# Performance work log

Hardware: AMD Instinct MI355X
Metric: run time of the kernel (lower is better)

Reference implementation:

```python
import jax, jax.numpy as jnp
import numpy as np

TOKENS, D_IN = 8192, 1024
E, D_OUT = 8, 1024
H = 2 * D_OUT  # Expert hidden = 2 * num_outputs


def setup_inputs() -> dict:
    key = jax.random.key(0)
    ks = jax.random.split(key, 4)
    s_in = 1.0 / np.sqrt(D_IN)
    s_h = 1.0 / np.sqrt(H)
    return {
        "x": jax.random.normal(ks[0], (TOKENS, D_IN), dtype=jnp.float32),
        "W1": jax.random.normal(ks[1], (E, D_IN, H), dtype=jnp.float32) * s_in,
        "b1": jnp.zeros((E, H), dtype=jnp.float32),
        "W2": jax.random.normal(ks[2], (E, H, D_OUT), dtype=jnp.float32) * s_h,
        "b2": jnp.zeros((E, D_OUT), dtype=jnp.float32),
        "Wg": jax.random.normal(ks[3], (D_IN, E), dtype=jnp.float32) * s_in,
        "bg": jnp.zeros((E,), dtype=jnp.float32),
    }


def reference(x, W1, b1, W2, b2, Wg, bg):
    # Gating: softmax over experts. gates: [N, E]
    gates = jax.nn.softmax(x @ Wg + bg, axis=-1)
    # All experts run densely: batched GEMM over expert axis.
    h = jax.nn.relu(jnp.einsum('nd,edh->neh', x, W1) + b1)       # [N, E, H]
    expert_out = jnp.einsum('neh,ehf->nef', h, W2) + b2          # [N, E, D_OUT]
    # Gate-weighted sum over experts (fused stack*gate->sum).
    return jnp.einsum('nef,ne->nf', expert_out, gates)            # [N, D_OUT]
```

## Files before the change

kernel.cpp:

```cpp
#include <hip/hip_runtime.h>
#include <stdint.h>

#define TOKENS 8192
#define D_IN   1024
#define NEXP   8
#define D_OUT  1024
#define HDIM   2048

typedef __bf16 bf16x8 __attribute__((ext_vector_type(8)));
typedef __bf16 bf16x4 __attribute__((ext_vector_type(4)));
typedef float  f32x4  __attribute__((ext_vector_type(4)));

__device__ __forceinline__ void gload16(const void* g, void* l) {
  __builtin_amdgcn_global_load_lds(
      (const __attribute__((address_space(1))) void*)g,
      (__attribute__((address_space(3))) void*)l,
      16, 0, 0);
}

template <int N>
__device__ __forceinline__ void waitv() {
  if constexpr (N == 0)      asm volatile("s_waitcnt vmcnt(0)" ::: "memory");
  else if constexpr (N == 1) asm volatile("s_waitcnt vmcnt(1)" ::: "memory");
  else if constexpr (N == 2) asm volatile("s_waitcnt vmcnt(2)" ::: "memory");
  else if constexpr (N == 3) asm volatile("s_waitcnt vmcnt(3)" ::: "memory");
  else if constexpr (N == 4) asm volatile("s_waitcnt vmcnt(4)" ::: "memory");
  else static_assert(N <= 4, "unsupported vmcnt");
}

__global__ void gate_cvt_kernel(const float* __restrict__ x,
                                const float* __restrict__ Wg,
                                const float* __restrict__ bg,
                                float* __restrict__ gates,
                                __bf16* __restrict__ xb) {
  const int lane = threadIdx.x & 63;
  const int n = blockIdx.x * 4 + (threadIdx.x >> 6);
  float acc[NEXP];
#pragma unroll
  for (int e = 0; e < NEXP; ++e) acc[e] = 0.f;
  const float* xr = x + (size_t)n * D_IN;
  __bf16* xo = xb + (size_t)n * D_IN;
#pragma unroll 4
  for (int d0 = 0; d0 < D_IN; d0 += 64) {
    const int d = d0 + lane;
    float xv = xr[d];
    xo[d] = (__bf16)xv;
    const float* wr = Wg + d * NEXP;
#pragma unroll
    for (int e = 0; e < NEXP; ++e) acc[e] += xv * wr[e];
  }
#pragma unroll
  for (int e = 0; e < NEXP; ++e) {
    float v = acc[e];
#pragma unroll
    for (int off = 32; off > 0; off >>= 1) v += __shfl_down(v, off);
    acc[e] = v;
  }
  if (lane == 0) {
    float mx = -1e30f;
#pragma unroll
    for (int e = 0; e < NEXP; ++e) { acc[e] += bg[e]; mx = fmaxf(mx, acc[e]); }
    float s = 0.f;
#pragma unroll
    for (int e = 0; e < NEXP; ++e) { acc[e] = expf(acc[e] - mx); s += acc[e]; }
    float inv = 1.f / s;
#pragma unroll
    for (int e = 0; e < NEXP; ++e) gates[n * NEXP + e] = acc[e] * inv;
  }
}

__global__ void transpose_cvt_kernel(const float* __restrict__ W,
                                     __bf16* __restrict__ Wt,
                                     int K, int N, int EPG) {
  __shared__ float tile[32][33];
  const int e = blockIdx.z;
  const int ldo = EPG * K;
  const float* Win = W + (size_t)e * K * N;
  __bf16* Wout = Wt + (size_t)(e / EPG) * N * ldo + (size_t)(e % EPG) * K;
  const int n0 = blockIdx.x * 32;
  const int k0 = blockIdx.y * 32;
  const int tx = threadIdx.x & 31;
  const int ty = threadIdx.x >> 5;
#pragma unroll
  for (int r = ty; r < 32; r += 8)
    tile[r][tx] = Win[(size_t)(k0 + r) * N + n0 + tx];
  __syncthreads();
#pragma unroll
  for (int r = ty; r < 32; r += 8)
    Wout[(size_t)(n0 + r) * ldo + k0 + tx] = (__bf16)tile[tx][r];
}

__global__ void merge_kernel(float* __restrict__ out,
                             const float* __restrict__ gates,
                             const float* __restrict__ b2) {
  const int idx = blockIdx.x * 256 + threadIdx.x;
  const int n = idx >> 8;
  const int fb = idx & 255;
  float4 o = ((const float4*)out)[idx];
  const float* g = gates + (size_t)n * NEXP;
#pragma unroll
  for (int e = 0; e < NEXP; ++e) {
    const float ge = g[e];
    float4 b = ((const float4*)(b2 + (size_t)e * D_OUT))[fb];
    o.x += ge * b.x; o.y += ge * b.y; o.z += ge * b.z; o.w += ge * b.w;
  }
  ((float4*)out)[idx] = o;
}

template <int NT, int WPE, int BM, int BN, int WM, int WN, int EPI>
__global__ __launch_bounds__(NT, WPE)
void moe_gemm(const __bf16* __restrict__ A, size_t AZ,
              const __bf16* __restrict__ B, size_t BZ,
              const float* __restrict__ b1g,
              const float* __restrict__ gates,
              int e0,
              __bf16* __restrict__ Hout, int OCZ, int ldo,
              float* __restrict__ F0,
              int first, int M, int N, int K) {
  constexpr int RM = BM / WM, RN = BN / WN;
  constexpr int FM = RM / 16, FN = RN / 16;
  constexpr int HM = FM / 2,  HN = FN / 2;
  constexpr int LA = BM * 4 / NT;
  constexpr int LB = BN * 4 / NT;
  constexpr int AELEM = BM * 64;
  static_assert(HM >= 1 && HN >= 1, "tile too small");
  __shared__ alignas(16) __bf16 lds[(BM + BN) * 64];

  const int tid  = threadIdx.x;
  const int lane = tid & 63;
  const int wave = tid >> 6;
  const int wr   = wave / WN;
  const int wc   = wave % WN;
  const int lrow = lane & 15;
  const int khi  = lane >> 4;
  const int sx   = (lrow & 7) << 3;
  const int bz   = blockIdx.z;

  A += (size_t)bz * AZ;
  B += (size_t)bz * BZ;

  const int Gx   = gridDim.x;
  const int nwg  = Gx * gridDim.y;
  const int orig = blockIdx.y * Gx + blockIdx.x;
  const int wgid = (orig & 7) * (nwg >> 3) + (orig >> 3);
  const int bn0  = (wgid % Gx) * BN;
  const int bm0  = (wgid / Gx) * BM;

  const __bf16* srcA[2][LA];
  const __bf16* srcB[2][LB];
#pragma unroll
  for (int q = 0; q < 2; ++q) {
#pragma unroll
    for (int j = 0; j < LA; ++j) {
      int o   = q * (BM * 64) + j * (NT * 16) + tid * 16;
      int row = o >> 7;
      int cb  = (o & 127) ^ ((row & 7) << 4);
      srcA[q][j] = A + (size_t)(bm0 + row) * K + (cb >> 1);
    }
#pragma unroll
    for (int j = 0; j < LB; ++j) {
      int o   = q * (BN * 64) + j * (NT * 16) + tid * 16;
      int row = o >> 7;
      int cb  = (o & 127) ^ ((row & 7) << 4);
      srcB[q][j] = B + (size_t)(bn0 + row) * K + (cb >> 1);
    }
  }

  auto stageA = [&](int kt, int q) {
#pragma unroll
    for (int j = 0; j < LA; ++j)
      gload16(srcA[q][j] + (size_t)kt * 64,
              lds + q * (BM * 32) + j * (NT * 8) + wave * 512);
  };
  auto stageB = [&](int kt, int q) {
#pragma unroll
    for (int j = 0; j < LB; ++j)
      gload16(srcB[q][j] + (size_t)kt * 64,
              lds + AELEM + q * (BN * 32) + j * (NT * 8) + wave * 512);
  };

  f32x4 acc[FM][FN];
#pragma unroll
  for (int m = 0; m < FM; ++m)
#pragma unroll
    for (int n = 0; n < FN; ++n) acc[m][n] = f32x4{0.f, 0.f, 0.f, 0.f};

  bf16x8 af[HM][2];
  bf16x8 bf[2][HN][2];

  auto rdA = [&](int mq) {
#pragma unroll
    for (int mi = 0; mi < HM; ++mi)
#pragma unroll
      for (int kk = 0; kk < 2; ++kk)
        af[mi][kk] = *(const bf16x8*)
            &lds[(size_t)(mq * (BM / 2) + wr * (RM / 2) + mi * 16 + lrow) * 64 +
                 ((kk * 32 + khi * 8) ^ sx)];
  };
  auto rdB = [&](int nq) {
#pragma unroll
    for (int ni = 0; ni < HN; ++ni)
#pragma unroll
      for (int kk = 0; kk < 2; ++kk)
        bf[nq][ni][kk] = *(const bf16x8*)
            &lds[AELEM +
                 (size_t)(nq * (BN / 2) + wc * (RN / 2) + ni * 16 + lrow) * 64 +
                 ((kk * 32 + khi * 8) ^ sx)];
  };
  auto cluster = [&](int mq, int nq) {
    __builtin_amdgcn_s_setprio(1);
#pragma unroll
    for (int kk = 0; kk < 2; ++kk)
#pragma unroll
      for (int mi = 0; mi < HM; ++mi)
#pragma unroll
        for (int ni = 0; ni < HN; ++ni)
          acc[mq * HM + mi][nq * HN + ni] =
              __builtin_amdgcn_mfma_f32_16x16x32_bf16(
                  af[mi][kk], bf[nq][ni][kk], acc[mq * HM + mi][nq * HN + ni],
                  0, 0, 0);
    __builtin_amdgcn_s_setprio(0);
  };

#define BAR()   asm volatile("s_barrier" ::: "memory")
#define LGKM0() do { asm volatile("s_waitcnt lgkmcnt(0)" ::: "memory"); \
                     __builtin_amdgcn_sched_barrier(0); } while (0)

  const int nk = K >> 6;

  stageA(0, 0); stageB(0, 0); stageB(0, 1);
  waitv<LB>();
  BAR();

  for (int t = 0; t < nk; ++t) {
    const bool pf = (t + 1 < nk);

    rdA(0); rdB(0);
    stageA(t, 1);
    BAR(); LGKM0();
    cluster(0, 0);
    waitv<LA>();
    BAR();
    rdB(1);
    if (pf) stageA(t + 1, 0);
    BAR(); LGKM0();
    cluster(0, 1);
    if (pf) waitv<LA>(); else waitv<0>();
    BAR();
    rdA(1);
    if (pf) stageB(t + 1, 0);
    BAR(); LGKM0();
    cluster(1, 0);
    BAR();
    if (pf) stageB(t + 1, 1);
    BAR();
    cluster(1, 1);
    if (pf) waitv<LB>();
    BAR();
  }

#undef BAR
#undef LGKM0

  const float* bias = (EPI == 0) ? b1g + (size_t)(e0 + bz) * HDIM : nullptr;
  const int ecol = e0 + bz;
  __bf16* Hp = (EPI == 0) ? Hout + (size_t)bz * OCZ : nullptr;

#pragma unroll
  for (int m = 0; m < FM; ++m) {
    const int grow0 = bm0 + (m / HM) * (BM / 2) + wr * (RM / 2) +
                      (m % HM) * 16 + khi * 4;
    if constexpr (EPI == 0) {
      float g[4];
#pragma unroll
      for (int r = 0; r < 4; ++r)
        g[r] = gates[(size_t)(grow0 + r) * NEXP + ecol];
#pragma unroll
      for (int n = 0; n < FN; ++n) {
        const int gcol = bn0 + (n / HN) * (BN / 2) + wc * (RN / 2) +
                         (n % HN) * 16 + lrow;
        const float bv = bias[gcol];
        f32x4 a = acc[m][n];
#pragma unroll
        for (int r = 0; r < 4; ++r) {
          float v = a[r] + bv;
          v = v > 0.f ? v : 0.f;
          Hp[(size_t)(grow0 + r) * ldo + gcol] = (__bf16)(v * g[r]);
        }
      }
    } else {
#pragma unroll
      for (int n = 0; n < FN; ++n) {
        const int gcol = bn0 + (n / HN) * (BN / 2) + wc * (RN / 2) +
                         (n % HN) * 16 + lrow;
        f32x4 a = acc[m][n];
#pragma unroll
        for (int r = 0; r < 4; ++r) {
          float* o = F0 + (size_t)(grow0 + r) * N + gcol;
          if (first) *o = a[r];
          else       *o += a[r];
        }
      }
    }
  }
}

extern "C" void kernel_launch(void* const* d_in, const int* in_sizes, int n_in,
                              void* d_out, int out_size, void* d_ws, size_t ws_size,
                              hipStream_t stream) {
  const float* x  = (const float*)d_in[0];
  const float* W1 = (const float*)d_in[1];
  const float* b1 = (const float*)d_in[2];
  const float* W2 = (const float*)d_in[3];
  const float* b2 = (const float*)d_in[4];
  const float* Wg = (const float*)d_in[5];
  const float* bg = (const float*)d_in[6];
  float* out = (float*)d_out;

  char* w = (char*)d_ws;
  float* gates = (float*)w;   w += (size_t)TOKENS * NEXP * 4;
  __bf16* xb   = (__bf16*)w;  w += (size_t)TOKENS * D_IN * 2;
  __bf16* w1t  = (__bf16*)w;  w += (size_t)NEXP * HDIM * D_IN * 2;
  __bf16* w2c  = (__bf16*)w;  w += (size_t)NEXP * D_OUT * HDIM * 2;
  const size_t base = (size_t)(w - (char*)d_ws);

  const size_t h1_b = (size_t)TOKENS * HDIM * 2;
  const int G = (ws_size >= base + 4 * h1_b) ? 4
              : (ws_size >= base + 2 * h1_b) ? 2 : 1;
  __bf16* hbuf = (__bf16*)w;

  const size_t WSLICE = (size_t)HDIM * D_IN;
  const int KB = G * HDIM;

  gate_cvt_kernel<<<TOKENS / 4, 256, 0, stream>>>(x, Wg, bg, gates, xb);
  transpose_cvt_kernel<<<dim3(HDIM / 32, D_IN / 32, NEXP), 256, 0, stream>>>(
      W1, w1t, D_IN, HDIM, 1);
  transpose_cvt_kernel<<<dim3(D_OUT / 32, HDIM / 32, NEXP), 256, 0, stream>>>(
      W2, w2c, HDIM, D_OUT, G);

  const int ngroups = NEXP / G;
  for (int d = 0; d < ngroups; ++d) {
    if (G >= 2) {
      for (int i2 = 0; i2 < G / 2; ++i2) {
        const int e0 = G * d + 2 * i2;
        moe_gemm<512, 2, 256, 256, 2, 4, 0><<<dim3(8, 32, 2), 512, 0, stream>>>(
            xb, 0, w1t + (size_t)e0 * WSLICE, WSLICE, b1, gates, e0,
            hbuf + (size_t)i2 * 2 * HDIM, HDIM, KB,
            nullptr, 0, TOKENS, HDIM, D_IN);
      }
    } else {
      moe_gemm<512, 2, 256, 256, 2, 4, 0><<<dim3(8, 32, 1), 512, 0, stream>>>(
          xb, 0, w1t + (size_t)d * WSLICE, 0, b1, gates, d,
          hbuf, 0, KB,
          nullptr, 0, TOKENS, HDIM, D_IN);
    }
    moe_gemm<256, 3, 128, 128, 2, 2, 3><<<dim3(D_OUT / 128, TOKENS / 128, 1),
                                          256, 0, stream>>>(
        hbuf, 0, w2c + (size_t)d * D_OUT * KB, 0,
        nullptr, nullptr, 0, nullptr, 0, 0,
        out, (d == 0) ? 1 : 0, TOKENS, D_OUT, KB);
  }

  merge_kernel<<<TOKENS, 256, 0, stream>>>(out, gates, b2);
}
```

Before: 645.5 us.

## Use register-staged double-buffered LDS pipeline for second MoE GEMM

Adds an RSTG variant of the GEMM used for the second (hidden-to-output) matmul. It loads tiles two k-steps ahead into registers and writes them into a double-buffered LDS slot, replacing direct global-to-LDS loads. This drops to one barrier per k-step instead of many. It also cuts that kernel's occupancy hint from 3 to 2 workgroups per CU, and the doubled LDS and extra registers (16 float4 staging values) may limit occupancy.

New measurement: 653.9 us. About the same (+1.3%).

```diff
diff --git a/kernel.cpp b/kernel.cpp
--- a/kernel.cpp
+++ b/kernel.cpp
@@ -25,7 +25,8 @@
   else if constexpr (N == 2) asm volatile("s_waitcnt vmcnt(2)" ::: "memory");
   else if constexpr (N == 3) asm volatile("s_waitcnt vmcnt(3)" ::: "memory");
   else if constexpr (N == 4) asm volatile("s_waitcnt vmcnt(4)" ::: "memory");
-  else static_assert(N <= 4, "unsupported vmcnt");
+  else if constexpr (N == 8) asm volatile("s_waitcnt vmcnt(8)" ::: "memory");
+  else static_assert(N <= 8, "unsupported vmcnt");
 }
 
 __global__ void gate_cvt_kernel(const float* __restrict__ x,
@@ -107,7 +108,7 @@
   ((float4*)out)[idx] = o;
 }
 
-template <int NT, int WPE, int BM, int BN, int WM, int WN, int EPI>
+template <int NT, int WPE, int BM, int BN, int WM, int WN, int EPI, int RSTG>
 __global__ __launch_bounds__(NT, WPE)
 void moe_gemm(const __bf16* __restrict__ A, size_t AZ,
               const __bf16* __restrict__ B, size_t BZ,
@@ -123,8 +124,10 @@
   constexpr int LA = BM * 4 / NT;
   constexpr int LB = BN * 4 / NT;
   constexpr int AELEM = BM * 64;
+  constexpr int SLOT  = (BM + BN) * 64;
+  constexpr int NSLOT = (RSTG == 0) ? 1 : 2;
   static_assert(HM >= 1 && HN >= 1, "tile too small");
-  __shared__ alignas(16) __bf16 lds[(BM + BN) * 64];
+  __shared__ alignas(16) __bf16 lds[NSLOT * SLOT];
 
   const int tid  = threadIdx.x;
   const int lane = tid & 63;
@@ -146,39 +149,6 @@
   const int bn0  = (wgid % Gx) * BN;
   const int bm0  = (wgid / Gx) * BM;
 
-  const __bf16* srcA[2][LA];
-  const __bf16* srcB[2][LB];
-#pragma unroll
-  for (int q = 0; q < 2; ++q) {
-#pragma unroll
-    for (int j = 0; j < LA; ++j) {
-      int o   = q * (BM * 64) + j * (NT * 16) + tid * 16;
-      int row = o >> 7;
-      int cb  = (o & 127) ^ ((row & 7) << 4);
-      srcA[q][j] = A + (size_t)(bm0 + row) * K + (cb >> 1);
-    }
-#pragma unroll
-    for (int j = 0; j < LB; ++j) {
-      int o   = q * (BN * 64) + j * (NT * 16) + tid * 16;
-      int row = o >> 7;
-      int cb  = (o & 127) ^ ((row & 7) << 4);
-      srcB[q][j] = B + (size_t)(bn0 + row) * K + (cb >> 1);
-    }
-  }
-
-  auto stageA = [&](int kt, int q) {
-#pragma unroll
-    for (int j = 0; j < LA; ++j)
-      gload16(srcA[q][j] + (size_t)kt * 64,
-              lds + q * (BM * 32) + j * (NT * 8) + wave * 512);
-  };
-  auto stageB = [&](int kt, int q) {
-#pragma unroll
-    for (int j = 0; j < LB; ++j)
-      gload16(srcB[q][j] + (size_t)kt * 64,
-              lds + AELEM + q * (BN * 32) + j * (NT * 8) + wave * 512);
-  };
-
   f32x4 acc[FM][FN];
 #pragma unroll
   for (int m = 0; m < FM; ++m)
@@ -188,24 +158,23 @@
   bf16x8 af[HM][2];
   bf16x8 bf[2][HN][2];
 
-  auto rdA = [&](int mq) {
+  auto rdA = [&](const __bf16* As, int mq) {
 #pragma unroll
     for (int mi = 0; mi < HM; ++mi)
 #pragma unroll
       for (int kk = 0; kk < 2; ++kk)
         af[mi][kk] = *(const bf16x8*)
-            &lds[(size_t)(mq * (BM / 2) + wr * (RM / 2) + mi * 16 + lrow) * 64 +
-                 ((kk * 32 + khi * 8) ^ sx)];
+            &As[(size_t)(mq * (BM / 2) + wr * (RM / 2) + mi * 16 + lrow) * 64 +
+                ((kk * 32 + khi * 8) ^ sx)];
   };
-  auto rdB = [&](int nq) {
+  auto rdB = [&](const __bf16* Bs, int nq) {
 #pragma unroll
     for (int ni = 0; ni < HN; ++ni)
 #pragma unroll
       for (int kk = 0; kk < 2; ++kk)
         bf[nq][ni][kk] = *(const bf16x8*)
-            &lds[AELEM +
-                 (size_t)(nq * (BN / 2) + wc * (RN / 2) + ni * 16 + lrow) * 64 +
-                 ((kk * 32 + khi * 8) ^ sx)];
+            &Bs[(size_t)(nq * (BN / 2) + wc * (RN / 2) + ni * 16 + lrow) * 64 +
+                ((kk * 32 + khi * 8) ^ sx)];
   };
   auto cluster = [&](int mq, int nq) {
     __builtin_amdgcn_s_setprio(1);
@@ -221,6 +190,22 @@
                   0, 0, 0);
     __builtin_amdgcn_s_setprio(0);
   };
+  auto cluster_h = [&](int mq) {
+    __builtin_amdgcn_s_setprio(1);
+#pragma unroll
+    for (int kk = 0; kk < 2; ++kk)
+#pragma unroll
+      for (int mi = 0; mi < HM; ++mi)
+#pragma unroll
+        for (int nq = 0; nq < 2; ++nq)
+#pragma unroll
+          for (int ni = 0; ni < HN; ++ni)
+            acc[mq * HM + mi][nq * HN + ni] =
+                __builtin_amdgcn_mfma_f32_16x16x32_bf16(
+                    af[mi][kk], bf[nq][ni][kk], acc[mq * HM + mi][nq * HN + ni],
+                    0, 0, 0);
+    __builtin_amdgcn_s_setprio(0);
+  };
 
 #define BAR()   asm volatile("s_barrier" ::: "memory")
 #define LGKM0() do { asm volatile("s_waitcnt lgkmcnt(0)" ::: "memory"); \
@@ -228,35 +213,154 @@
 
   const int nk = K >> 6;
 
-  stageA(0, 0); stageB(0, 0); stageB(0, 1);
-  waitv<LB>();
-  BAR();
-
-  for (int t = 0; t < nk; ++t) {
-    const bool pf = (t + 1 < nk);
-
-    rdA(0); rdB(0);
-    stageA(t, 1);
-    BAR(); LGKM0();
-    cluster(0, 0);
-    waitv<LA>();
+  if constexpr (RSTG == 0) {
+    const __bf16* srcA[2][LA];
+    const __bf16* srcB[2][LB];
+#pragma unroll
+    for (int q = 0; q < 2; ++q) {
+#pragma unroll
+      for (int j = 0; j < LA; ++j) {
+        int o   = q * (BM * 64) + j * (NT * 16) + tid * 16;
+        int row = o >> 7;
+        int cb  = (o & 127) ^ ((row & 7) << 4);
+        srcA[q][j] = A + (size_t)(bm0 + row) * K + (cb >> 1);
+      }
+#pragma unroll
+      for (int j = 0; j < LB; ++j) {
+        int o   = q * (BN * 64) + j * (NT * 16) + tid * 16;
+        int row = o >> 7;
+        int cb  = (o & 127) ^ ((row & 7) << 4);
+        srcB[q][j] = B + (size_t)(bn0 + row) * K + (cb >> 1);
+      }
+    }
+    auto stageA = [&](int kt, int q) {
+#pragma unroll
+      for (int j = 0; j < LA; ++j)
+        gload16(srcA[q][j] + (size_t)kt * 64,
+                lds + q * (BM * 32) + j * (NT * 8) + wave * 512);
+    };
+    auto stageB = [&](int kt, int q) {
+#pragma unroll
+      for (int j = 0; j < LB; ++j)
+        gload16(srcB[q][j] + (size_t)kt * 64,
+                lds + AELEM + q * (BN * 32) + j * (NT * 8) + wave * 512);
+    };
+
+    stageA(0, 0); stageB(0, 0); stageB(0, 1);
+    waitv<LB>();
     BAR();
-    rdB(1);
-    if (pf) stageA(t + 1, 0);
-    BAR(); LGKM0();
-    cluster(0, 1);
-    if (pf) waitv<LA>(); else waitv<0>();
+    for (int t = 0; t < nk; ++t) {
+      const bool pf = (t + 1 < nk);
+      rdA(lds, 0); rdB(lds + AELEM, 0);
+      stageA(t, 1);
+      BAR(); LGKM0();
+      cluster(0, 0);
+      waitv<LA>();
+      BAR();
+      rdB(lds + AELEM, 1);
+      if (pf) stageA(t + 1, 0);
+      BAR(); LGKM0();
+      cluster(0, 1);
+      if (pf) waitv<LA>(); else waitv<0>();
+      BAR();
+      rdA(lds, 1);
+      if (pf) stageB(t + 1, 0);
+      BAR(); LGKM0();
+      cluster(1, 0);
+      BAR();
+      if (pf) stageB(t + 1, 1);
+      BAR();
+      cluster(1, 1);
+      if (pf) waitv<LB>();
+      BAR();
+    }
+  } else {
+    static_assert(LA == 2 && LB == 2, "RSTG sized for 128x128 @256 thr");
+    const __bf16 *sl0, *sl1, *sl2, *sl3, *sl4, *sl5, *sl6, *sl7;
+    int dz0, dz1, dz2, dz3, dz4, dz5, dz6, dz7;
+#define MKSRC(i, SL, DZ)                                                       \
+  do {                                                                         \
+    int o    = (i) * (NT * 16) + tid * 16;                                     \
+    bool isA = (o < BM * 128);                                                 \
+    int oo   = isA ? o : (o - BM * 128);                                       \
+    int row  = oo >> 7;                                                        \
+    int cbl  = oo & 127;                                                       \
+    SL = (isA ? A + (size_t)(bm0 + row) * K                                    \
+              : B + (size_t)(bn0 + row) * K) + (cbl >> 1);                     \
+    DZ = (isA ? 0 : BM * 128) + ((oo & ~127) | (cbl ^ ((row & 7) << 4)));      \
+  } while (0)
+    MKSRC(0, sl0, dz0); MKSRC(1, sl1, dz1); MKSRC(2, sl2, dz2);
+    MKSRC(3, sl3, dz3); MKSRC(4, sl4, dz4); MKSRC(5, sl5, dz5);
+    MKSRC(6, sl6, dz6); MKSRC(7, sl7, dz7);
+#undef MKSRC
+
+    float4 SA0, SA1, SA2, SA3, SA4, SA5, SA6, SA7;
+    float4 SB0, SB1, SB2, SB3, SB4, SB5, SB6, SB7;
+#define ISSUE8(kt, P)                                                          \
+  do {                                                                         \
+    P##0 = *(const float4*)(sl0 + (size_t)(kt) * 64);                          \
+    P##1 = *(const float4*)(sl1 + (size_t)(kt) * 64);                          \
+    P##2 = *(const float4*)(sl2 + (size_t)(kt) * 64);                          \
+    P##3 = *(const float4*)(sl3 + (size_t)(kt) * 64);                          \
+    P##4 = *(const float4*)(sl4 + (size_t)(kt) * 64);                          \
+    P##5 = *(const float4*)(sl5 + (size_t)(kt) * 64);                          \
+    P##6 = *(const float4*)(sl6 + (size_t)(kt) * 64);                          \
+    P##7 = *(const float4*)(sl7 + (size_t)(kt) * 64);                          \
+  } while (0)
+#define WST8(sbyte, P)                                                         \
+  do {                                                                         \
+    char* b_ = (char*)lds + (sbyte);                                           \
+    *(float4*)(b_ + dz0) = P##0; *(float4*)(b_ + dz1) = P##1;                  \
+    *(float4*)(b_ + dz2) = P##2; *(float4*)(b_ + dz3) = P##3;                  \
+    *(float4*)(b_ + dz4) = P##4; *(float4*)(b_ + dz5) = P##5;                  \
+    *(float4*)(b_ + dz6) = P##6; *(float4*)(b_ + dz7) = P##7;                  \
+  } while (0)
+
+    ISSUE8(0, SA);
+    ISSUE8(1, SB);
+    waitv<8>();
+    WST8(0, SA);
+    LGKM0();
     BAR();
-    rdA(1);
-    if (pf) stageB(t + 1, 0);
-    BAR(); LGKM0();
-    cluster(1, 0);
-    BAR();
-    if (pf) stageB(t + 1, 1);
-    BAR();
-    cluster(1, 1);
-    if (pf) waitv<LB>();
-    BAR();
+
+    const int half = nk >> 1;
+    for (int tt = 0; tt < half; ++tt) {
+      {
+        const int t = 2 * tt;
+        const __bf16* As = lds;
+        const __bf16* Bs = lds + AELEM;
+        const bool pf2 = (t + 2 < nk);
+        rdA(As, 0); rdB(Bs, 0); rdB(Bs, 1);
+        if (pf2) ISSUE8(t + 2, SA);
+        LGKM0();
+        cluster_h(0);
+        rdA(As, 1);
+        if (pf2) waitv<8>(); else waitv<0>();
+        WST8(SLOT * 2, SB);
+        LGKM0();
+        cluster_h(1);
+        BAR();
+      }
+      {
+        const int t = 2 * tt + 1;
+        const __bf16* As = lds + SLOT;
+        const __bf16* Bs = As + AELEM;
+        const bool pf2 = (t + 2 < nk);
+        const bool pf1 = (t + 1 < nk);
+        rdA(As, 0); rdB(Bs, 0); rdB(Bs, 1);
+        if (pf2) ISSUE8(t + 2, SB);
+        LGKM0();
+        cluster_h(0);
+        rdA(As, 1);
+        if (pf2) waitv<8>(); else if (pf1) waitv<0>();
+        if (pf1) WST8(0, SA);
+        LGKM0();
+        cluster_h(1);
+        BAR();
+      }
+    }
+#undef ISSUE8
+#undef WST8
   }
 
 #undef BAR
@@ -343,19 +447,21 @@
     if (G >= 2) {
       for (int i2 = 0; i2 < G / 2; ++i2) {
         const int e0 = G * d + 2 * i2;
-        moe_gemm<512, 2, 256, 256, 2, 4, 0><<<dim3(8, 32, 2), 512, 0, stream>>>(
+        moe_gemm<512, 2, 256, 256, 2, 4, 0, 0>
+            <<<dim3(8, 32, 2), 512, 0, stream>>>(
             xb, 0, w1t + (size_t)e0 * WSLICE, WSLICE, b1, gates, e0,
             hbuf + (size_t)i2 * 2 * HDIM, HDIM, KB,
             nullptr, 0, TOKENS, HDIM, D_IN);
       }
     } else {
-      moe_gemm<512, 2, 256, 256, 2, 4, 0><<<dim3(8, 32, 1), 512, 0, stream>>>(
+      moe_gemm<512, 2, 256, 256, 2, 4, 0, 0>
+          <<<dim3(8, 32, 1), 512, 0, stream>>>(
           xb, 0, w1t + (size_t)d * WSLICE, 0, b1, gates, d,
           hbuf, 0, KB,
           nullptr, 0, TOKENS, HDIM, D_IN);
     }
-    moe_gemm<256, 3, 128, 128, 2, 2, 3><<<dim3(D_OUT / 128, TOKENS / 128, 1),
-                                          256, 0, stream>>>(
+    moe_gemm<256, 2, 128, 128, 2, 2, 3, 1>
+        <<<dim3(D_OUT / 128, TOKENS / 128, 1), 256, 0, stream>>>(
         hbuf, 0, w2c + (size_t)d * D_OUT * KB, 0,
         nullptr, nullptr, 0, nullptr, 0, 0,
         out, (d == 0) ? 1 : 0, TOKENS, D_OUT, KB);
```
